# Optimization experiments

Hardware: AMD Instinct MI355X
Metric: run time of the kernel (lower is better)

## Reference

```python
import jax, jax.numpy as jnp
import numpy as np

Q, T, N = 1024, 256, 100
EPS = 1e-6


def setup_inputs() -> dict:
    key = jax.random.key(0)
    ks = jax.random.split(key, 8)
    return {
        'pred_curve_points': jax.random.normal(ks[0], (1, Q, N, 3), jnp.float32),
        'pred_curve_logits': jax.random.normal(ks[1], (1, Q, 2), jnp.float32),
        'pred_curve_type': jax.random.normal(ks[2], (1, Q, 4), jnp.float32),
        'closed_curve_logits': jax.random.normal(ks[3], (1, Q, 2), jnp.float32),
        'tgt_curve_points': jax.random.normal(ks[4], (T, N, 3), jnp.float32),
        'tgt_labels': jax.random.randint(ks[5], (T,), 0, 4, jnp.int64),
        'tgt_is_closed': jax.random.randint(ks[6], (T,), 0, 2, jnp.int64),
        'curve_length_weighting': jax.random.uniform(ks[7], (T,), jnp.float32),
    }


def reference(pred_curve_points, pred_curve_logits, pred_curve_type,
              closed_curve_logits, tgt_curve_points, tgt_labels,
              tgt_is_closed, curve_length_weighting):
    preds = pred_curve_points[0]                       # [Q,N,3] (batch_size=1)
    q, n, _ = preds.shape
    t = tgt_curve_points.shape[0]

    type_prob = jax.nn.softmax(pred_curve_type[0], axis=-1)      # [Q,4]
    valid_prob = jax.nn.softmax(pred_curve_logits[0], axis=-1)   # [Q,2]
    closed_prob = jax.nn.softmax(closed_curve_logits[0], axis=-1)  # [Q,2]

    # classification cost [Q,T]
    cost_class = (-jnp.log(type_prob[:, tgt_labels] + EPS)
                  - jnp.log(valid_prob[:, 0:1] + EPS)
                  - jnp.log(closed_prob[:, tgt_is_closed] + EPS))

    # cyclic variants of each target curve: all rolls of fwd + reversed orders
    j = jnp.arange(n)
    R = (j[None, :] - j[:, None]) % n                  # R[k, j] = (j-k) % n
    v_fwd = tgt_curve_points[:, R, :]                  # [T,N,N,3]
    v_bwd = tgt_curve_points[:, ::-1, :][:, R, :]      # [T,N,N,3]
    variants = jnp.concatenate([v_fwd, v_bwd], axis=1).reshape(t, 2 * n, 3 * n)
    preds_flat = preds.reshape(q, 3 * n)

    # squared cdist on flattened curves / n  (|a|^2 + |b|^2 - 2 a.b)
    ab = jnp.einsum('tvd,qd->tvq', variants, preds_flat)
    v2 = jnp.sum(tgt_curve_points ** 2, axis=(1, 2))[:, None, None]
    p2 = jnp.sum(preds_flat ** 2, axis=1)[None, None, :]
    d2 = jnp.maximum(v2 + p2 - 2.0 * ab, 0.0) / n      # [T,2N,Q]

    # closed curves: min over all 2N cyclic variants, remap reversed ids
    closed_d = d2.min(axis=1)                          # [T,Q]
    closed_ids = jnp.argmin(d2, axis=1)
    closed_ids = jnp.where(closed_ids > n - 1, 2 * n - 1 - closed_ids, closed_ids)
    # open curves: min over identity (variant 0) and full reversal (variant N)
    open_d = jnp.minimum(d2[:, 0], d2[:, n])           # [T,Q]

    is_closed_b = (tgt_is_closed > 0)[:, None]
    geom = jnp.where(is_closed_b, closed_d, open_d).T  # [Q,T]
    ids = jnp.where(is_closed_b, closed_ids, 0).T.astype(jnp.int32)

    geom = geom * curve_length_weighting[None, :]
    C = 1.0 * geom + 1.0 * cost_class                  # cost_position=cost_class=1
    return C, ids
```

## Files before the change

kernel.cpp:

```cpp
#include <hip/hip_runtime.h>
#include <hip/hip_fp16.h>

#define Q_TOT 1024
#define T_TOT 256
#define NPTS  100
#define KD    300
#define EPSV  1e-6f

#define KSTEPS 10
#define EXTOFF 40
#define EXTLEN 672

typedef _Float16 f16;
typedef _Float16 f16x8 __attribute__((ext_vector_type(8)));
typedef float    f32x4 __attribute__((ext_vector_type(4)));
#define MFMA16 __builtin_amdgcn_mfma_f32_16x16x32_f16

#define WS_PF 1280

__global__ __launch_bounds__(256) void prep_all(const float* __restrict__ preds,
                                                const float* __restrict__ tgt,
                                                float* __restrict__ ws)
{
    __shared__ __align__(16) float ext[16][308];
    const int b   = blockIdx.x;
    const int tid = threadIdx.x;

    {
        const float4* src = (const float4*)(preds + b*16*KD);
        for (int i = tid; i < 1200; i += 256) {
            int row = i / 75;
            int c   = i - row*75;
            *(float4*)&ext[row][c*4] = src[i];
        }
    }
    __syncthreads();

    f16x8* pf = (f16x8*)(ws + WS_PF) + b*1280;
    for (int j = tid; j < 1280; j += 256) {
        int lane = j & 63;
        int r    = j >> 6;
        int s    = r & 1;
        int ks   = r >> 1;
        int qr   = lane & 15;
        int kb   = ks*32 + (lane >> 4)*8;
        f16x8 v;
        #pragma unroll
        for (int jj = 0; jj < 8; ++jj) {
            int k = kb + jj;
            float x = (k < KD) ? ext[qr][k] : 0.f;
            f16 h = (f16)x;
            v[jj] = s ? (f16)(x - (float)h) : h;
        }
        pf[j] = v;
    }

    const int wv   = tid >> 6;
    const int lane = tid & 63;
    #pragma unroll
    for (int rr = 0; rr < 4; ++rr) {
        int row = wv*4 + rr;
        float s = 0.f;
        for (int k = lane; k < KD; k += 64) s = fmaf(ext[row][k], ext[row][k], s);
        #pragma unroll
        for (int m = 1; m < 64; m <<= 1) s += __shfl_xor(s, m, 64);
        if (lane == 0) ws[b*16 + row] = s;
    }
    {
        const float* base = tgt + (b*4 + wv)*KD;
        float s = 0.f;
        for (int k = lane; k < KD; k += 64) s = fmaf(base[k], base[k], s);
        #pragma unroll
        for (int m = 1; m < 64; m <<= 1) s += __shfl_xor(s, m, 64);
        if (lane == 0) ws[1024 + b*4 + wv] = s;
    }
}

template<int MTB, int NMT>
__device__ __forceinline__ void sweep(const f16 (*sext)[8][EXTLEN],
                                      const f16x8* __restrict__ pfrag,
                                      int ntg0, int lane, int col, int rg, int cA,
                                      float v2t, const float (&p2v)[4],
                                      float (&minD)[4], int (&minI)[4],
                                      float (*sopen)[512], int ntl0)
{
    f32x4 acc[NMT][4];
    #pragma unroll
    for (int h = 0; h < NMT; ++h)
        #pragma unroll
        for (int nt = 0; nt < 4; ++nt) acc[h][nt] = (f32x4){0.f,0.f,0.f,0.f};

    #pragma clang loop unroll(disable)
    for (int ks = 0; ks < KSTEPS; ++ks) {
        f16x8 ah[NMT], alo[NMT];
        #pragma unroll
        for (int h = 0; h < NMT; ++h) {
            const int mt  = MTB + h;
            const int mtp = (mt < 7) ? mt : mt-7;
            const int sel = (mt < 7) ? 0 : 2;
            const int idx = EXTOFF + 300 - 48*mtp - 3*col + 8*rg - cA + 32*ks;
            ah[h]  = *(const f16x8*)&sext[sel  ][cA][idx];
            alo[h] = *(const f16x8*)&sext[sel+1][cA][idx];
        }
        #pragma unroll
        for (int nt = 0; nt < 4; ++nt) {
            const int fi = ((ntg0+nt)*KSTEPS + ks)*128 + lane;
            f16x8 bh = pfrag[fi];
            f16x8 bl = pfrag[fi + 64];
            #pragma unroll
            for (int h = 0; h < NMT; ++h) {
                acc[h][nt] = MFMA16(ah[h],  bh, acc[h][nt], 0,0,0);
                acc[h][nt] = MFMA16(ah[h],  bl, acc[h][nt], 0,0,0);
                acc[h][nt] = MFMA16(alo[h], bh, acc[h][nt], 0,0,0);
            }
        }
    }

    #pragma unroll
    for (int h = 0; h < NMT; ++h) {
        const int mt   = MTB + h;
        const int mtp  = (mt < 7) ? mt : mt-7;
        const int voff = (mt < 7) ? 0 : 100;
        const int ab   = mtp*16 + rg*4;
        #pragma unroll
        for (int nt = 0; nt < 4; ++nt) {
            const float s2 = v2t + p2v[nt];
            #pragma unroll
            for (int r = 0; r < 4; ++r) {
                const int al = ab + r;
                if (al < 100) {
                    float d2 = fmaxf(fmaf(-2.f, acc[h][nt][r], s2), 0.f) * 0.01f;
                    int vlog = voff + al;
                    if (d2 < minD[nt]) { minD[nt] = d2; minI[nt] = vlog; }
                    if (al == 0) sopen[voff ? 1 : 0][(ntl0+nt)*16 + col] = d2;
                }
            }
        }
    }
}

__global__ __launch_bounds__(512) void matcher_mfma(
    const float* __restrict__ ws,
    const float* __restrict__ tgt,
    const float* __restrict__ plog,
    const float* __restrict__ ptyp,
    const float* __restrict__ clog,
    const int*   __restrict__ labels,
    const int*   __restrict__ iscl,
    const float* __restrict__ clw,
    float* __restrict__ out)
{
    __shared__ __align__(16) f16 sext[4][8][EXTLEN];
    __shared__ float redD[2048];
    __shared__ int   redI[2048];
    __shared__ float sopen[2][512];

    const int t    = blockIdx.x;
    const int nb   = blockIdx.y;
    const int tid  = threadIdx.x;
    const int lane = tid & 63;
    const int w    = tid >> 6;
    const int col  = lane & 15;
    const int rg   = lane >> 4;
    const int ntl0 = w*4;
    const int ntg0 = nb*32 + ntl0;

    const float* tg = tgt + t*KD;
    for (int x = tid; x < EXTLEN; x += 512) {
        int e = x - EXTOFF;
        float vF = 0.f, vR = 0.f;
        if (e >= 0 && e < 600) {
            int m = (e >= 300) ? e - 300 : e;
            vF = tg[m];
            int jj = m / 3, c3 = m - 3*jj;
            vR = tg[(NPTS-1-jj)*3 + c3];
        }
        f16 fh = (f16)vF, fl = (f16)(vF - (float)fh);
        f16 rh = (f16)vR, rl = (f16)(vR - (float)rh);
        #pragma unroll
        for (int c = 0; c < 8; ++c) {
            int y = x - c;
            if (y >= 0) {
                sext[0][c][y] = fh; sext[1][c][y] = fl;
                sext[2][c][y] = rh; sext[3][c][y] = rl;
            }
        }
    }

    const float v2t = ws[1024 + t];
    float p2v[4];
    #pragma unroll
    for (int nt = 0; nt < 4; ++nt) p2v[nt] = ws[(ntg0+nt)*16 + col];
    const f16x8* __restrict__ pfrag = (const f16x8*)(ws + WS_PF);
    const int cA = (EXTOFF + 300 - 3*col) & 7;
    __syncthreads();

    float minD[4]; int minI[4];
    #pragma unroll
    for (int nt = 0; nt < 4; ++nt) { minD[nt] = 3.4028235e38f; minI[nt] = 0; }

    sweep< 0,4>(sext, pfrag, ntg0, lane, col, rg, cA, v2t, p2v, minD, minI, sopen, ntl0);
    sweep< 4,4>(sext, pfrag, ntg0, lane, col, rg, cA, v2t, p2v, minD, minI, sopen, ntl0);
    sweep< 8,4>(sext, pfrag, ntg0, lane, col, rg, cA, v2t, p2v, minD, minI, sopen, ntl0);
    sweep<12,2>(sext, pfrag, ntg0, lane, col, rg, cA, v2t, p2v, minD, minI, sopen, ntl0);

    #pragma unroll
    for (int nt = 0; nt < 4; ++nt) {
        redD[(ntl0+nt)*64 + lane] = minD[nt];
        redI[(ntl0+nt)*64 + lane] = minI[nt];
    }
    __syncthreads();

    {
        const int lq   = tid;
        const int tile = lq >> 4;
        const int cc   = lq & 15;
        const int base = tile*64 + cc;
        float bd = redD[base]; int bi = redI[base];
        #pragma unroll
        for (int g = 1; g < 4; ++g) {
            float d = redD[base + g*16]; int i = redI[base + g*16];
            if (d < bd || (d == bd && i < bi)) { bd = d; bi = i; }
        }
        const int q = nb*512 + lq;
        int mapped = (bi <= NPTS-1) ? bi : (2*NPTS-1 - bi);
        float od   = fminf(sopen[0][lq], sopen[1][lq]);
        int   isc  = iscl[t];
        float geom = isc ? bd : od;
        int   ido  = isc ? mapped : 0;
        geom *= clw[t];

        float t0 = ptyp[q*4+0], t1 = ptyp[q*4+1];
        float t2 = ptyp[q*4+2], t3 = ptyp[q*4+3];
        float mx = fmaxf(fmaxf(t0,t1), fmaxf(t2,t3));
        float e0 = expf(t0-mx), e1 = expf(t1-mx), e2 = expf(t2-mx), e3 = expf(t3-mx);
        float rs = 1.0f/(e0+e1+e2+e3);
        int lab  = labels[t];
        float el = (lab == 0) ? e0 : (lab == 1) ? e1 : (lab == 2) ? e2 : e3;
        float cost = -logf(el*rs + EPSV);
        float v0 = plog[q*2+0], v1 = plog[q*2+1];
        cost += -logf(1.0f/(1.0f + expf(v1-v0)) + EPSV);
        float c0 = clog[q*2+0], c1 = clog[q*2+1];
        float pc = isc ? (1.0f/(1.0f + expf(c0-c1))) : (1.0f/(1.0f + expf(c1-c0)));
        cost += -logf(pc + EPSV);

        float C = geom + cost;
        out[q*T_TOT + t]               = C;
        out[Q_TOT*T_TOT + q*T_TOT + t] = (float)ido;
    }
}

extern "C" void kernel_launch(void* const* d_in, const int* in_sizes, int n_in,
                              void* d_out, int out_size, void* d_ws, size_t ws_size,
                              hipStream_t stream)
{
    const float* preds  = (const float*)d_in[0];
    const float* plog   = (const float*)d_in[1];
    const float* ptyp   = (const float*)d_in[2];
    const float* clog   = (const float*)d_in[3];
    const float* tgt    = (const float*)d_in[4];
    const int*   labels = (const int*)d_in[5];
    const int*   iscl   = (const int*)d_in[6];
    const float* clw    = (const float*)d_in[7];
    float* out = (float*)d_out;
    float* ws  = (float*)d_ws;

    prep_all    <<<dim3(64),       dim3(256), 0, stream>>>(preds, tgt, ws);
    matcher_mfma<<<dim3(T_TOT, 2), dim3(512), 0, stream>>>(
        ws, tgt, plog, ptyp, clog, labels, iscl, clw, out);
}
```

Before: 173.2 us.

## Halve per-block query tiles, sweep all variants per direction, double grid

Each warp now handles 2 query tiles instead of 4 and sweeps all 7 variant tiles per direction (forward, then reversed) in one pass. The grid doubles along the query axis to 4 blocks per target. Loads of the hi and lo A fragments are split into separate phases to cut live registers. This aims to raise occupancy and parallelism, at the cost of reading each target's LDS extension twice as often, rebuilding it in twice as many blocks, and leaving half the threads idle in the final reduction.

Result: faster. 161.8 us (-6.6%).

```diff
diff --git a/kernel.cpp b/kernel.cpp
--- a/kernel.cpp
+++ b/kernel.cpp
@@ -76,63 +76,76 @@
     }
 }
 
-template<int MTB, int NMT>
-__device__ __forceinline__ void sweep(const f16 (*sext)[8][EXTLEN],
-                                      const f16x8* __restrict__ pfrag,
-                                      int ntg0, int lane, int col, int rg, int cA,
-                                      float v2t, const float (&p2v)[4],
-                                      float (&minD)[4], int (&minI)[4],
-                                      float (*sopen)[512], int ntl0)
-{
-    f32x4 acc[NMT][4];
-    #pragma unroll
-    for (int h = 0; h < NMT; ++h)
-        #pragma unroll
-        for (int nt = 0; nt < 4; ++nt) acc[h][nt] = (f32x4){0.f,0.f,0.f,0.f};
+template<int SEL, int VOFF>
+__device__ __forceinline__ void sweep2(const f16 (*sext)[8][EXTLEN],
+                                       const f16x8* __restrict__ pfrag,
+                                       int ntg0, int lane, int col, int rg, int cA,
+                                       float v2t, const float (&p2v)[2],
+                                       float (&minD)[2], int (&minI)[2],
+                                       float (*sopen)[256], int ntl0)
+{
+    f32x4 acc[7][2];
+    #pragma unroll
+    for (int h = 0; h < 7; ++h)
+        #pragma unroll
+        for (int nt = 0; nt < 2; ++nt) acc[h][nt] = (f32x4){0.f,0.f,0.f,0.f};
 
     #pragma clang loop unroll(disable)
     for (int ks = 0; ks < KSTEPS; ++ks) {
-        f16x8 ah[NMT], alo[NMT];
-        #pragma unroll
-        for (int h = 0; h < NMT; ++h) {
-            const int mt  = MTB + h;
-            const int mtp = (mt < 7) ? mt : mt-7;
-            const int sel = (mt < 7) ? 0 : 2;
-            const int idx = EXTOFF + 300 - 48*mtp - 3*col + 8*rg - cA + 32*ks;
-            ah[h]  = *(const f16x8*)&sext[sel  ][cA][idx];
-            alo[h] = *(const f16x8*)&sext[sel+1][cA][idx];
-        }
-        #pragma unroll
-        for (int nt = 0; nt < 4; ++nt) {
+        f16x8 bh[2], bl[2];
+        #pragma unroll
+        for (int nt = 0; nt < 2; ++nt) {
             const int fi = ((ntg0+nt)*KSTEPS + ks)*128 + lane;
-            f16x8 bh = pfrag[fi];
-            f16x8 bl = pfrag[fi + 64];
-            #pragma unroll
-            for (int h = 0; h < NMT; ++h) {
-                acc[h][nt] = MFMA16(ah[h],  bh, acc[h][nt], 0,0,0);
-                acc[h][nt] = MFMA16(ah[h],  bl, acc[h][nt], 0,0,0);
-                acc[h][nt] = MFMA16(alo[h], bh, acc[h][nt], 0,0,0);
-            }
-        }
-    }
-
-    #pragma unroll
-    for (int h = 0; h < NMT; ++h) {
-        const int mt   = MTB + h;
-        const int mtp  = (mt < 7) ? mt : mt-7;
-        const int voff = (mt < 7) ? 0 : 100;
-        const int ab   = mtp*16 + rg*4;
-        #pragma unroll
-        for (int nt = 0; nt < 4; ++nt) {
+            bh[nt] = pfrag[fi];
+            bl[nt] = pfrag[fi + 64];
+        }
+        {
+            f16x8 ah[7];
+            #pragma unroll
+            for (int h = 0; h < 7; ++h) {
+                const int idx = EXTOFF + 300 - 48*h - 3*col + 8*rg - cA + 32*ks;
+                ah[h] = *(const f16x8*)&sext[SEL][cA][idx];
+            }
+            #pragma unroll
+            for (int nt = 0; nt < 2; ++nt)
+                #pragma unroll
+                for (int h = 0; h < 7; ++h)
+                    acc[h][nt] = MFMA16(ah[h], bh[nt], acc[h][nt], 0,0,0);
+            #pragma unroll
+            for (int nt = 0; nt < 2; ++nt)
+                #pragma unroll
+                for (int h = 0; h < 7; ++h)
+                    acc[h][nt] = MFMA16(ah[h], bl[nt], acc[h][nt], 0,0,0);
+        }
+        {
+            f16x8 alo[7];
+            #pragma unroll
+            for (int h = 0; h < 7; ++h) {
+                const int idx = EXTOFF + 300 - 48*h - 3*col + 8*rg - cA + 32*ks;
+                alo[h] = *(const f16x8*)&sext[SEL+1][cA][idx];
+            }
+            #pragma unroll
+            for (int nt = 0; nt < 2; ++nt)
+                #pragma unroll
+                for (int h = 0; h < 7; ++h)
+                    acc[h][nt] = MFMA16(alo[h], bh[nt], acc[h][nt], 0,0,0);
+        }
+    }
+
+    #pragma unroll
+    for (int h = 0; h < 7; ++h) {
+        const int ab = h*16 + rg*4;
+        #pragma unroll
+        for (int nt = 0; nt < 2; ++nt) {
             const float s2 = v2t + p2v[nt];
             #pragma unroll
             for (int r = 0; r < 4; ++r) {
                 const int al = ab + r;
                 if (al < 100) {
                     float d2 = fmaxf(fmaf(-2.f, acc[h][nt][r], s2), 0.f) * 0.01f;
-                    int vlog = voff + al;
+                    int vlog = VOFF + al;
                     if (d2 < minD[nt]) { minD[nt] = d2; minI[nt] = vlog; }
-                    if (al == 0) sopen[voff ? 1 : 0][(ntl0+nt)*16 + col] = d2;
+                    if (al == 0) sopen[VOFF ? 1 : 0][(ntl0+nt)*16 + col] = d2;
                 }
             }
         }
@@ -151,9 +164,9 @@
     float* __restrict__ out)
 {
     __shared__ __align__(16) f16 sext[4][8][EXTLEN];
-    __shared__ float redD[2048];
-    __shared__ int   redI[2048];
-    __shared__ float sopen[2][512];
+    __shared__ float redD[1024];
+    __shared__ int   redI[1024];
+    __shared__ float sopen[2][256];
 
     const int t    = blockIdx.x;
     const int nb   = blockIdx.y;
@@ -162,8 +175,8 @@
     const int w    = tid >> 6;
     const int col  = lane & 15;
     const int rg   = lane >> 4;
-    const int ntl0 = w*4;
-    const int ntg0 = nb*32 + ntl0;
+    const int ntl0 = w*2;
+    const int ntg0 = nb*16 + ntl0;
 
     const float* tg = tgt + t*KD;
     for (int x = tid; x < EXTLEN; x += 512) {
@@ -188,30 +201,28 @@
     }
 
     const float v2t = ws[1024 + t];
-    float p2v[4];
-    #pragma unroll
-    for (int nt = 0; nt < 4; ++nt) p2v[nt] = ws[(ntg0+nt)*16 + col];
+    float p2v[2];
+    #pragma unroll
+    for (int nt = 0; nt < 2; ++nt) p2v[nt] = ws[(ntg0+nt)*16 + col];
     const f16x8* __restrict__ pfrag = (const f16x8*)(ws + WS_PF);
     const int cA = (EXTOFF + 300 - 3*col) & 7;
     __syncthreads();
 
-    float minD[4]; int minI[4];
-    #pragma unroll
-    for (int nt = 0; nt < 4; ++nt) { minD[nt] = 3.4028235e38f; minI[nt] = 0; }
-
-    sweep< 0,4>(sext, pfrag, ntg0, lane, col, rg, cA, v2t, p2v, minD, minI, sopen, ntl0);
-    sweep< 4,4>(sext, pfrag, ntg0, lane, col, rg, cA, v2t, p2v, minD, minI, sopen, ntl0);
-    sweep< 8,4>(sext, pfrag, ntg0, lane, col, rg, cA, v2t, p2v, minD, minI, sopen, ntl0);
-    sweep<12,2>(sext, pfrag, ntg0, lane, col, rg, cA, v2t, p2v, minD, minI, sopen, ntl0);
-
-    #pragma unroll
-    for (int nt = 0; nt < 4; ++nt) {
+    float minD[2]; int minI[2];
+    #pragma unroll
+    for (int nt = 0; nt < 2; ++nt) { minD[nt] = 3.4028235e38f; minI[nt] = 0; }
+
+    sweep2<0,  0>(sext, pfrag, ntg0, lane, col, rg, cA, v2t, p2v, minD, minI, sopen, ntl0);
+    sweep2<2,100>(sext, pfrag, ntg0, lane, col, rg, cA, v2t, p2v, minD, minI, sopen, ntl0);
+
+    #pragma unroll
+    for (int nt = 0; nt < 2; ++nt) {
         redD[(ntl0+nt)*64 + lane] = minD[nt];
         redI[(ntl0+nt)*64 + lane] = minI[nt];
     }
     __syncthreads();
 
-    {
+    if (tid < 256) {
         const int lq   = tid;
         const int tile = lq >> 4;
         const int cc   = lq & 15;
@@ -222,7 +233,7 @@
             float d = redD[base + g*16]; int i = redI[base + g*16];
             if (d < bd || (d == bd && i < bi)) { bd = d; bi = i; }
         }
-        const int q = nb*512 + lq;
+        const int q = nb*256 + lq;
         int mapped = (bi <= NPTS-1) ? bi : (2*NPTS-1 - bi);
         float od   = fminf(sopen[0][lq], sopen[1][lq]);
         int   isc  = iscl[t];
@@ -266,6 +277,6 @@
     float* ws  = (float*)d_ws;
 
     prep_all    <<<dim3(64),       dim3(256), 0, stream>>>(preds, tgt, ws);
-    matcher_mfma<<<dim3(T_TOT, 2), dim3(512), 0, stream>>>(
+    matcher_mfma<<<dim3(T_TOT, 4), dim3(512), 0, stream>>>(
         ws, tgt, plog, ptyp, clog, labels, iscl, clw, out);
 }
```
